# Kernel tuning notes

Hardware: AMD Instinct MI355X
Metric: run time of the kernel (lower is better)

## Reference

```python
import jax, jax.numpy as jnp
import numpy as np

GROUP = 64      # int4 quantization group size
QMAX = 7.0      # symmetric int4 grid [-8, 7], scales from max/7
EPS = 1e-6      # RMSNorm epsilon


def fake_quant_int4(t, group=GROUP):
    """Symmetric per-group int4 fake-quantization along the last dim (STE)."""
    shp = t.shape
    g = t.reshape(shp[:-1] + (shp[-1] // group, group))
    s = jnp.maximum(jnp.max(jnp.abs(g), axis=-1, keepdims=True) / QMAX, 1e-8)
    q = jnp.clip(jnp.round(g / s), -8.0, 7.0) * s
    out = g + jax.lax.stop_gradient(q - g)  # straight-through
    return out.reshape(shp)


def rms_norm(x, w):
    var = jnp.mean(jnp.square(x), axis=-1, keepdims=True)
    return x * jax.lax.rsqrt(var + EPS) * w


def apply_rope(x, cos, sin):
    # x: [B,S,H,D]; cos/sin: [S, D//2]; rotate consecutive pairs (complex mult)
    xr = x.reshape(x.shape[:-1] + (x.shape[-1] // 2, 2))
    a, b = xr[..., 0], xr[..., 1]
    c = cos[None, :, None, :]
    s = sin[None, :, None, :]
    out = jnp.stack([a * c - b * s, a * s + b * c], axis=-1)
    return out.reshape(x.shape)


def setup_inputs() -> dict:
    B, S, C, OUT, R, D = 2, 4096, 3072, 9216, 32, 128
    key = jax.random.key(0)
    ks = jax.random.split(key, 6)
    x = jax.random.normal(ks[0], (B, S, C), jnp.float32)
    smooth = jax.random.uniform(ks[1], (C,), jnp.float32, minval=0.5, maxval=1.5)
    weight = jax.random.normal(ks[2], (OUT, C), jnp.float32) * 0.02
    proj_down = jax.random.normal(ks[3], (C, R), jnp.float32) * 0.02
    proj_up = jax.random.normal(ks[4], (OUT, R), jnp.float32) * 0.02
    bias = jax.random.normal(ks[5], (OUT,), jnp.float32) * 0.01
    norm_q_weight = jnp.ones((D,), jnp.float32)
    norm_k_weight = jnp.ones((D,), jnp.float32)
    half = D // 2
    inv_freq = 1.0 / (10000.0 ** (jnp.arange(half, dtype=jnp.float32) / half))
    ang = jnp.arange(S, dtype=jnp.float32)[:, None] * inv_freq[None, :]
    return {
        "x": x, "smooth": smooth, "weight": weight,
        "proj_down": proj_down, "proj_up": proj_up, "bias": bias,
        "norm_q_weight": norm_q_weight, "norm_k_weight": norm_k_weight,
        "freqs_cos": jnp.cos(ang), "freqs_sin": jnp.sin(ang),
    }


def reference(x, smooth, weight, proj_down, proj_up, bias,
              norm_q_weight, norm_k_weight, freqs_cos, freqs_sin):
    B, S, C = x.shape
    OUT = weight.shape[0]
    D = norm_q_weight.shape[0]
    H = (OUT // 3) // D
    # --- svdq_quantize_w4a4_act_fuse_lora: smooth, lora-down, int4 quantize ---
    xs = x.reshape(B * S, C) / smooth                 # smoothed activations
    lora_act = xs @ proj_down                          # [BS, R]
    xq = fake_quant_int4(xs)                           # per-token group-64 int4
    # --- svdq_gemm_w4a4: int4 GEMM + LoRA-up + bias epilogue ---
    wq = fake_quant_int4(weight)                       # per-row group-64 int4
    out = xq @ wq.T + lora_act @ proj_up.T + bias      # [BS, OUT]
    out = out.reshape(B, S, 3, H, D)                   # q,k,v concat order
    q, k, v = out[:, :, 0], out[:, :, 1], out[:, :, 2]
    # --- fused RMSNorm + RoPE epilogue on q and k ---
    q = apply_rope(rms_norm(q, norm_q_weight), freqs_cos, freqs_sin)
    k = apply_rope(rms_norm(k, norm_k_weight), freqs_cos, freqs_sin)
    return jnp.concatenate(
        [q.reshape(B, S, -1), k.reshape(B, S, -1), v.reshape(B, S, -1)], axis=-1)
```

## Files before the change

kernel.cpp:

```cpp
#include <hip/hip_runtime.h>

#define CDIM  3072
#define MROWS 8192
#define NOUT  9216
#define NW    24

typedef __bf16 bf16x8 __attribute__((ext_vector_type(8)));
typedef float f32x4 __attribute__((ext_vector_type(4)));
typedef int i32x4 __attribute__((ext_vector_type(4)));

__device__ __forceinline__ unsigned short f2bf(float f) {
  union { float f; unsigned int u; } v; v.f = f;
  unsigned int u = v.u;
  return (unsigned short)((u + 0x7fffu + ((u >> 16) & 1u)) >> 16);
}
__device__ __forceinline__ float bfu_lo(unsigned int u) {
  union { unsigned int v; float f; } x; x.v = u << 16; return x.f;
}
__device__ __forceinline__ float bfu_hi(unsigned int u) {
  union { unsigned int v; float f; } x; x.v = u & 0xffff0000u; return x.f;
}
__device__ __forceinline__ void gld16(const void* g, void* l) {
  __builtin_amdgcn_global_load_lds(
      (const __attribute__((address_space(1))) void*)g,
      (__attribute__((address_space(3))) void*)l, 16, 0, 0);
}

#define BARRIER() asm volatile("s_barrier" ::: "memory")
#define LGKM0()   asm volatile("s_waitcnt lgkmcnt(0)" ::: "memory")

template<int N> __device__ __forceinline__ void vmw() {
  if constexpr (N == 8)      asm volatile("s_waitcnt vmcnt(8)" ::: "memory");
  else if constexpr (N == 4) asm volatile("s_waitcnt vmcnt(4)" ::: "memory");
  else if constexpr (N == 0) asm volatile("s_waitcnt vmcnt(0)" ::: "memory");
}

__device__ __forceinline__ unsigned int requant4(unsigned int u, float f) {
  const int q0 = (int)(signed char)(u & 0xff);
  const int q1 = (int)(signed char)((u >> 8) & 0xff);
  const int q2 = (int)(signed char)((u >> 16) & 0xff);
  const int q3 = (int)(signed char)(u >> 24);
  const int r0 = (int)rintf((float)q0 * f);
  const int r1 = (int)rintf((float)q1 * f);
  const int r2 = (int)rintf((float)q2 * f);
  const int r3 = (int)rintf((float)q3 * f);
  return (r0 & 0xff) | ((r1 & 0xff) << 8) | ((r2 & 0xff) << 16)
       | ((unsigned int)(r3 & 0xff) << 24);
}

__global__ __launch_bounds__(256) void k_prep(
    const float* __restrict__ wt, const float* __restrict__ pu,
    const float* __restrict__ x, const float* __restrict__ smooth,
    const float* __restrict__ pd,
    signed char* __restrict__ Bq, float* __restrict__ Sb_r,
    unsigned short* __restrict__ Blor,
    signed char* __restrict__ Aq, float* __restrict__ Sa_r,
    unsigned short* __restrict__ Alor) {
  __shared__ unsigned short xsb[4][3072];
  __shared__ float plds[4][32][33];
  __shared__ float sred[4];
  const int tid = threadIdx.x;

  if (blockIdx.x < NOUT) {
    const int row = blockIdx.x;
    unsigned int u[3]; float sl[3];
    #pragma unroll
    for (int it = 0; it < 3; ++it) {
      const int c = it * 1024 + tid * 4;
      const float4 v = *(const float4*)&wt[(size_t)row * CDIM + c];
      float am = fmaxf(fmaxf(fabsf(v.x), fabsf(v.y)), fmaxf(fabsf(v.z), fabsf(v.w)));
      #pragma unroll
      for (int off = 1; off < 16; off <<= 1) am = fmaxf(am, __shfl_xor(am, off));
      const float s = fmaxf(am / 7.0f, 1e-8f);
      union { signed char c[4]; unsigned int u; } pk;
      pk.c[0] = (signed char)(int)fminf(fmaxf(rintf(v.x / s), -8.f), 7.f);
      pk.c[1] = (signed char)(int)fminf(fmaxf(rintf(v.y / s), -8.f), 7.f);
      pk.c[2] = (signed char)(int)fminf(fmaxf(rintf(v.z / s), -8.f), 7.f);
      pk.c[3] = (signed char)(int)fminf(fmaxf(rintf(v.w / s), -8.f), 7.f);
      u[it] = pk.u; sl[it] = s;
    }
    float smax = fmaxf(fmaxf(sl[0], sl[1]), sl[2]);
    #pragma unroll
    for (int off = 16; off < 64; off <<= 1) smax = fmaxf(smax, __shfl_xor(smax, off));
    if ((tid & 63) == 0) sred[tid >> 6] = smax;
    __syncthreads();
    const float S = fmaxf(fmaxf(sred[0], sred[1]), fmaxf(sred[2], sred[3]));
    const float inv16 = 16.0f / S;
    #pragma unroll
    for (int it = 0; it < 3; ++it) {
      const int c = it * 1024 + tid * 4;
      *(unsigned int*)&Bq[(size_t)row * CDIM + c] = requant4(u[it], sl[it] * inv16);
    }
    if (tid == 0) Sb_r[row] = S * 0.0625f;
    if (tid < 32) Blor[row * 32 + tid] = f2bf(pu[row * 32 + tid]);
    return;
  }

  const int blk = blockIdx.x - NOUT;
  const int w = tid >> 6, l = tid & 63;
  const int row = blk * 4 + w;
  const float* xr = x + (size_t)row * CDIM;
  unsigned int u[12]; float sl[12];

  #pragma unroll
  for (int it = 0; it < 12; ++it) {
    const int c = it * 256 + l * 4;
    const float4 xv = *(const float4*)&xr[c];
    const float4 sm = *(const float4*)&smooth[c];
    float4 xs;
    xs.x = xv.x / sm.x; xs.y = xv.y / sm.y;
    xs.z = xv.z / sm.z; xs.w = xv.w / sm.w;
    ushort4 xb;
    xb.x = f2bf(xs.x); xb.y = f2bf(xs.y); xb.z = f2bf(xs.z); xb.w = f2bf(xs.w);
    *(ushort4*)&xsb[w][c] = xb;
    float am = fmaxf(fmaxf(fabsf(xs.x), fabsf(xs.y)), fmaxf(fabsf(xs.z), fabsf(xs.w)));
    #pragma unroll
    for (int off = 1; off < 16; off <<= 1) am = fmaxf(am, __shfl_xor(am, off));
    const float s = fmaxf(am / 7.0f, 1e-8f);
    union { signed char c[4]; unsigned int u; } pk;
    pk.c[0] = (signed char)(int)fminf(fmaxf(rintf(xs.x / s), -8.f), 7.f);
    pk.c[1] = (signed char)(int)fminf(fmaxf(rintf(xs.y / s), -8.f), 7.f);
    pk.c[2] = (signed char)(int)fminf(fmaxf(rintf(xs.z / s), -8.f), 7.f);
    pk.c[3] = (signed char)(int)fminf(fmaxf(rintf(xs.w / s), -8.f), 7.f);
    u[it] = pk.u; sl[it] = s;
  }
  float smax = sl[0];
  #pragma unroll
  for (int it = 1; it < 12; ++it) smax = fmaxf(smax, sl[it]);
  #pragma unroll
  for (int off = 16; off < 64; off <<= 1) smax = fmaxf(smax, __shfl_xor(smax, off));
  const float S = smax;
  const float inv16 = 16.0f / S;
  #pragma unroll
  for (int it = 0; it < 12; ++it) {
    const int c = it * 256 + l * 4;
    *(unsigned int*)&Aq[(size_t)row * CDIM + c] = requant4(u[it], sl[it] * inv16);
  }
  if (l == 0) Sa_r[row] = S * 0.0625f;
  __syncthreads();

  const int ch = tid >> 3, rg = tid & 7;
  float acc[4][4] = {};
  for (int i = 0; i < 48; ++i) {
    const int c = ch * 2 + i * 64;
    const float4 p0 = *(const float4*)&pd[(size_t)c * 32 + rg * 4];
    const float4 p1 = *(const float4*)&pd[(size_t)(c + 1) * 32 + rg * 4];
    #pragma unroll
    for (int r4 = 0; r4 < 4; ++r4) {
      const unsigned int uu = *(const unsigned int*)&xsb[r4][c];
      const float xa = bfu_lo(uu), xb = bfu_hi(uu);
      acc[r4][0] += xa * p0.x + xb * p1.x;
      acc[r4][1] += xa * p0.y + xb * p1.y;
      acc[r4][2] += xa * p0.z + xb * p1.z;
      acc[r4][3] += xa * p0.w + xb * p1.w;
    }
  }
  #pragma unroll
  for (int r4 = 0; r4 < 4; ++r4)
    #pragma unroll
    for (int jj = 0; jj < 4; ++jj)
      plds[r4][rg * 4 + jj][ch] = acc[r4][jj];
  __syncthreads();
  if (tid < 128) {
    const int rr = tid >> 5, r = tid & 31;
    float ssum = 0.f;
    #pragma unroll
    for (int cc = 0; cc < 32; ++cc) ssum += plds[rr][r][cc];
    Alor[(size_t)(blk * 4 + rr) * 32 + r] = f2bf(ssum);
  }
}

template<int VM1, int VM3, int DO01, int DO23>
__device__ __forceinline__ void gemm_window(
    char* lds, i32x4 (&acc)[8][4],
    const signed char* Asrc, const signed char* Bsrc,
    int tid, int arow, int brow, int fsb, int par, int t) {
  const int A0 = par * 16384;
  const int A1 = 32768 + par * 16384;
  const int B0 = 65536 + par * 16384;
  const int B1 = 98304 + par * 16384;
  const int A1n = 32768 + (par ^ 1) * 16384;
  const int B1n = 98304 + (par ^ 1) * 16384;
  i32x4 a[4], b[4];

  #pragma unroll
  for (int ni = 0; ni < 4; ++ni) b[ni] = *(const i32x4*)(lds + B0 + (brow + ni * 16) * 64 + fsb);
  #pragma unroll
  for (int mi = 0; mi < 4; ++mi) a[mi] = *(const i32x4*)(lds + A0 + (arow + mi * 16) * 64 + fsb);
  if (DO01) {
    const int kc = (t + 1) * 128 + 64;
    gld16(Asrc + kc, lds + A1n + tid * 16);
    gld16(Asrc + (size_t)128 * CDIM + kc, lds + A1n + 8192 + tid * 16);
  }
  BARRIER(); LGKM0();
  __builtin_amdgcn_s_setprio(1);
  #pragma unroll
  for (int mi = 0; mi < 4; ++mi)
    #pragma unroll
    for (int ni = 0; ni < 4; ++ni)
      acc[mi][ni] = __builtin_amdgcn_mfma_i32_16x16x64_i8(a[mi], b[ni], acc[mi][ni], 0, 0, 0);
  __builtin_amdgcn_s_setprio(0);
  BARRIER();

  #pragma unroll
  for (int mi = 0; mi < 4; ++mi) a[mi] = *(const i32x4*)(lds + A0 + (arow + 64 + mi * 16) * 64 + fsb);
  if (DO01) {
    const int kc = (t + 1) * 128 + 64;
    gld16(Bsrc + kc, lds + B1n + tid * 16);
    gld16(Bsrc + (size_t)128 * CDIM + kc, lds + B1n + 8192 + tid * 16);
  }
  BARRIER(); LGKM0();
  __builtin_amdgcn_s_setprio(1);
  #pragma unroll
  for (int mi = 0; mi < 4; ++mi)
    #pragma unroll
    for (int ni = 0; ni < 4; ++ni)
      acc[4 + mi][ni] = __builtin_amdgcn_mfma_i32_16x16x64_i8(a[mi], b[ni], acc[4 + mi][ni], 0, 0, 0);
  __builtin_amdgcn_s_setprio(0);
  vmw<VM1>();
  BARRIER();

  #pragma unroll
  for (int ni = 0; ni < 4; ++ni) b[ni] = *(const i32x4*)(lds + B1 + (brow + ni * 16) * 64 + fsb);
  #pragma unroll
  for (int mi = 0; mi < 4; ++mi) a[mi] = *(const i32x4*)(lds + A1 + (arow + mi * 16) * 64 + fsb);
  if (DO23) {
    const int kc = (t + 2) * 128;
    gld16(Asrc + kc, lds + A0 + tid * 16);
    gld16(Asrc + (size_t)128 * CDIM + kc, lds + A0 + 8192 + tid * 16);
  }
  BARRIER(); LGKM0();
  __builtin_amdgcn_s_setprio(1);
  #pragma unroll
  for (int mi = 0; mi < 4; ++mi)
    #pragma unroll
    for (int ni = 0; ni < 4; ++ni)
      acc[mi][ni] = __builtin_amdgcn_mfma_i32_16x16x64_i8(a[mi], b[ni], acc[mi][ni], 0, 0, 0);
  __builtin_amdgcn_s_setprio(0);
  BARRIER();

  #pragma unroll
  for (int mi = 0; mi < 4; ++mi) a[mi] = *(const i32x4*)(lds + A1 + (arow + 64 + mi * 16) * 64 + fsb);
  if (DO23) {
    const int kc = (t + 2) * 128;
    gld16(Bsrc + kc, lds + B0 + tid * 16);
    gld16(Bsrc + (size_t)128 * CDIM + kc, lds + B0 + 8192 + tid * 16);
  }
  BARRIER(); LGKM0();
  __builtin_amdgcn_s_setprio(1);
  #pragma unroll
  for (int mi = 0; mi < 4; ++mi)
    #pragma unroll
    for (int ni = 0; ni < 4; ++ni)
      acc[4 + mi][ni] = __builtin_amdgcn_mfma_i32_16x16x64_i8(a[mi], b[ni], acc[4 + mi][ni], 0, 0, 0);
  __builtin_amdgcn_s_setprio(0);
  vmw<VM3>();
  BARRIER();
}

__global__ __launch_bounds__(512, 2) void k_gemmi8(
    const signed char* __restrict__ Aq, const signed char* __restrict__ Bq,
    const float* __restrict__ Sa_r, const float* __restrict__ Sb_r,
    const unsigned short* __restrict__ Alor, const unsigned short* __restrict__ Blor,
    const float* __restrict__ bias,
    const float* __restrict__ nqw, const float* __restrict__ nkw,
    const float* __restrict__ fcos, const float* __restrict__ fsin,
    float* __restrict__ outp) {
  __shared__ char lds[131072];
  const int tid = threadIdx.x;
  const int w = tid >> 6, l = tid & 63;
  const int wr = w >> 2, wc = w & 3;
  const int l16 = l & 15, g16 = l >> 4;
  const int xcd = blockIdx.x & 7;
  const int jj = blockIdx.x >> 3;
  const int chunk = jj / 36;
  const int tt = jj - chunk * 36;
  const int by = xcd * 4 + tt / 9;
  const int bx = chunk * 9 + tt % 9;
  const int n0 = bx * 256, m0 = by * 256;
  const int arow = wr * 128 + l16;
  const int brow = wc * 64 + l16;
  const int fsb = (g16 ^ ((l16 >> 1) & 3)) << 4;
  const int sr = tid >> 2;
  const int ss = (((tid & 3) ^ ((sr >> 1) & 3)) << 4);
  const signed char* Asrc = Aq + (size_t)(m0 + sr) * CDIM + ss;
  const signed char* Bsrc = Bq + (size_t)(n0 + sr) * CDIM + ss;
  i32x4 acc[8][4] = {};

  gld16(Asrc, lds + tid * 16);                  gld16(Asrc + (size_t)128 * CDIM, lds + 8192 + tid * 16);
  gld16(Bsrc, lds + 65536 + tid * 16);          gld16(Bsrc + (size_t)128 * CDIM, lds + 73728 + tid * 16);
  gld16(Asrc + 64, lds + 32768 + tid * 16);     gld16(Asrc + (size_t)128 * CDIM + 64, lds + 40960 + tid * 16);
  gld16(Bsrc + 64, lds + 98304 + tid * 16);     gld16(Bsrc + (size_t)128 * CDIM + 64, lds + 106496 + tid * 16);
  gld16(Asrc + 128, lds + 16384 + tid * 16);    gld16(Asrc + (size_t)128 * CDIM + 128, lds + 24576 + tid * 16);
  gld16(Bsrc + 128, lds + 81920 + tid * 16);    gld16(Bsrc + (size_t)128 * CDIM + 128, lds + 90112 + tid * 16);
  vmw<8>(); BARRIER();

  #pragma unroll 1
  for (int t = 0; t <= NW - 3; ++t)
    gemm_window<8, 8, 1, 1>(lds, acc, Asrc, Bsrc, tid, arow, brow, fsb, t & 1, t);
  gemm_window<8, 4, 1, 0>(lds, acc, Asrc, Bsrc, tid, arow, brow, fsb, (NW - 2) & 1, NW - 2);
  gemm_window<0, 63, 0, 0>(lds, acc, Asrc, Bsrc, tid, arow, brow, fsb, (NW - 1) & 1, NW - 1);

  {
    const char* Al0 = (const char*)Alor + (size_t)(m0 + sr) * 64 + ss;
    const char* Bl0 = (const char*)Blor + (size_t)(n0 + sr) * 64 + ss;
    gld16(Al0, lds + tid * 16);            gld16(Al0 + 128 * 64, lds + 8192 + tid * 16);
    gld16(Bl0, lds + 65536 + tid * 16);    gld16(Bl0 + 128 * 64, lds + 73728 + tid * 16);
  }

  f32x4 facc[8][4];
  float sbv[4];
  #pragma unroll
  for (int ni = 0; ni < 4; ++ni) sbv[ni] = Sb_r[n0 + wc * 64 + ni * 16 + l16];
  #pragma unroll
  for (int q = 0; q < 8; ++q) {
    const f32x4 sa4 = *(const f32x4*)&Sa_r[m0 + wr * 128 + q * 16 + g16 * 4];
    #pragma unroll
    for (int ni = 0; ni < 4; ++ni)
      facc[q][ni] = __builtin_convertvector(acc[q][ni], f32x4) * (sa4 * sbv[ni]);
  }

  vmw<0>(); BARRIER();
  {
    bf16x8 bl[4];
    #pragma unroll
    for (int ni = 0; ni < 4; ++ni)
      bl[ni] = *(const bf16x8*)(lds + 65536 + (brow + ni * 16) * 64 + fsb);
    #pragma unroll
    for (int q = 0; q < 8; ++q) {
      const bf16x8 al = *(const bf16x8*)(lds + (arow + q * 16) * 64 + fsb);
      #pragma unroll
      for (int ni = 0; ni < 4; ++ni)
        facc[q][ni] = __builtin_amdgcn_mfma_f32_16x16x32_bf16(al, bl[ni], facc[q][ni], 0, 0, 0);
    }
  }

  float bvv[4];
  #pragma unroll
  for (int ni = 0; ni < 4; ++ni) bvv[ni] = bias[n0 + wc * 64 + ni * 16 + l16];
  #pragma unroll
  for (int q = 0; q < 8; ++q)
    #pragma unroll
    for (int ni = 0; ni < 4; ++ni)
      #pragma unroll
      for (int j = 0; j < 4; ++j) facc[q][ni][j] += bvv[ni];

  if (n0 < 6144) {
    const float* nwt = (n0 < 3072) ? nqw : nkw;
    float nw[4];
    #pragma unroll
    for (int ni = 0; ni < 4; ++ni) nw[ni] = nwt[(wc & 1) * 64 + ni * 16 + l16];

    float part[8][4];
    #pragma unroll
    for (int q = 0; q < 8; ++q)
      #pragma unroll
      for (int j = 0; j < 4; ++j) {
        float ssum = 0.f;
        #pragma unroll
        for (int ni = 0; ni < 4; ++ni) ssum += facc[q][ni][j] * facc[q][ni][j];
        #pragma unroll
        for (int off = 1; off < 16; off <<= 1) ssum += __shfl_xor(ssum, off);
        part[q][j] = ssum;
      }

    __syncthreads();
    float* sq = (float*)lds;
    if (l16 == 0) {
      #pragma unroll
      for (int q = 0; q < 8; ++q)
        #pragma unroll
        for (int j = 0; j < 4; ++j) {
          const int r128 = q * 16 + g16 * 4 + j;
          sq[(((wr * 128 + r128) * 2 + (wc >> 1)) * 2) + (wc & 1)] = part[q][j];
        }
    }
    __syncthreads();

    #pragma unroll
    for (int q = 0; q < 8; ++q) {
      #pragma unroll
      for (int j = 0; j < 4; ++j) {
        const int r128 = q * 16 + g16 * 4 + j;
        const float other = sq[(((wr * 128 + r128) * 2 + (wc >> 1)) * 2) + ((wc & 1) ^ 1)];
        const float rinv = 1.0f / sqrtf((part[q][j] + other) * (1.0f / 128.0f) + 1e-6f);
        const int row = m0 + wr * 128 + r128;
        const int sidx = row & 4095;
        #pragma unroll
        for (int ni = 0; ni < 4; ++ni) {
          const int p = (wc & 1) * 32 + ni * 8 + (l16 >> 1);
          const float cv = fcos[(size_t)sidx * 64 + p];
          const float sv = fsin[(size_t)sidx * 64 + p];
          const float v = facc[q][ni][j] * rinv * nw[ni];
          const float o = __shfl_xor(v, 1);
          const float res = ((l & 1) == 0) ? (v * cv - o * sv) : (o * sv + v * cv);
          __builtin_nontemporal_store(res, &outp[(size_t)row * NOUT + n0 + wc * 64 + ni * 16 + l16]);
        }
      }
    }
  } else {
    #pragma unroll
    for (int ni = 0; ni < 4; ++ni) {
      const int gn = n0 + wc * 64 + ni * 16 + l16;
      #pragma unroll
      for (int q = 0; q < 8; ++q) {
        const int gm = m0 + wr * 128 + q * 16 + g16 * 4;
        #pragma unroll
        for (int j = 0; j < 4; ++j)
          __builtin_nontemporal_store(facc[q][ni][j], &outp[(size_t)(gm + j) * NOUT + gn]);
      }
    }
  }
}

extern "C" void kernel_launch(void* const* d_in, const int* in_sizes, int n_in,
                              void* d_out, int out_size, void* d_ws, size_t ws_size,
                              hipStream_t stream) {
  const float* x      = (const float*)d_in[0];
  const float* smooth = (const float*)d_in[1];
  const float* weight = (const float*)d_in[2];
  const float* pd     = (const float*)d_in[3];
  const float* pu     = (const float*)d_in[4];
  const float* bias   = (const float*)d_in[5];
  const float* nqw    = (const float*)d_in[6];
  const float* nkw    = (const float*)d_in[7];
  const float* fcos   = (const float*)d_in[8];
  const float* fsin   = (const float*)d_in[9];
  float* out = (float*)d_out;

  char* ws = (char*)d_ws;
  signed char* Aq   = (signed char*)ws;
  signed char* Bq   = (signed char*)(ws + 25165824);
  float* Sa_r       = (float*)(ws + 53477376);
  float* Sb_r       = (float*)(ws + 53510144);
  unsigned short* Alor = (unsigned short*)(ws + 53547008);
  unsigned short* Blor = (unsigned short*)(ws + 54071296);

  k_prep<<<dim3(NOUT + MROWS / 4), dim3(256), 0, stream>>>(
      weight, pu, x, smooth, pd, Bq, Sb_r, Blor, Aq, Sa_r, Alor);
  k_gemmi8<<<dim3(1152), dim3(512), 0, stream>>>(Aq, Bq, Sa_r, Sb_r, Alor, Blor,
                                                 bias, nqw, nkw, fcos, fsin, out);
}
```

Measured before the change: 369.2 us.

## Restructure int8 GEMM main loop into two-phase double-buffered windows

The four-phase K window with staggered partial prefetches and `vmcnt(8)` waits is replaced by a two-phase window. Each phase reads both 64-wide K sub-tiles from LDS and issues two MFMAs per accumulator. All eight next-tile global loads are issued up front and drained with `vmcnt(0)` at the end of the window. The LoRA A/B tile loads are folded into the last window's prefetch slot. This halves the barriers per window and removes the separate epilogue wait, but the prefetch distance shrinks and the doubled a/b operand arrays raise register pressure.

Result: slower. 389.0 us (+5.4%).

```diff
diff --git a/kernel.cpp b/kernel.cpp
--- a/kernel.cpp
+++ b/kernel.cpp
@@ -30,9 +30,7 @@
 #define LGKM0()   asm volatile("s_waitcnt lgkmcnt(0)" ::: "memory")
 
 template<int N> __device__ __forceinline__ void vmw() {
-  if constexpr (N == 8)      asm volatile("s_waitcnt vmcnt(8)" ::: "memory");
-  else if constexpr (N == 4) asm volatile("s_waitcnt vmcnt(4)" ::: "memory");
-  else if constexpr (N == 0) asm volatile("s_waitcnt vmcnt(0)" ::: "memory");
+  if constexpr (N == 0) asm volatile("s_waitcnt vmcnt(0)" ::: "memory");
 }
 
 __device__ __forceinline__ unsigned int requant4(unsigned int u, float f) {
@@ -170,91 +168,75 @@
   }
 }
 
-template<int VM1, int VM3, int DO01, int DO23>
-__device__ __forceinline__ void gemm_window(
+__device__ __forceinline__ void gemm_window2(
     char* lds, i32x4 (&acc)[8][4],
     const signed char* Asrc, const signed char* Bsrc,
-    int tid, int arow, int brow, int fsb, int par, int t) {
+    const char* AlorP, const char* BlorP,
+    int tid, int arow, int brow, int fsb, int par, int t, int mode) {
   const int A0 = par * 16384;
   const int A1 = 32768 + par * 16384;
   const int B0 = 65536 + par * 16384;
   const int B1 = 98304 + par * 16384;
+  const int A0n = (par ^ 1) * 16384;
   const int A1n = 32768 + (par ^ 1) * 16384;
+  const int B0n = 65536 + (par ^ 1) * 16384;
   const int B1n = 98304 + (par ^ 1) * 16384;
-  i32x4 a[4], b[4];
-
-  #pragma unroll
-  for (int ni = 0; ni < 4; ++ni) b[ni] = *(const i32x4*)(lds + B0 + (brow + ni * 16) * 64 + fsb);
-  #pragma unroll
-  for (int mi = 0; mi < 4; ++mi) a[mi] = *(const i32x4*)(lds + A0 + (arow + mi * 16) * 64 + fsb);
-  if (DO01) {
-    const int kc = (t + 1) * 128 + 64;
-    gld16(Asrc + kc, lds + A1n + tid * 16);
-    gld16(Asrc + (size_t)128 * CDIM + kc, lds + A1n + 8192 + tid * 16);
+  i32x4 a[8], b[8];
+
+  #pragma unroll
+  for (int ni = 0; ni < 4; ++ni) {
+    b[ni]     = *(const i32x4*)(lds + B0 + (brow + ni * 16) * 64 + fsb);
+    b[4 + ni] = *(const i32x4*)(lds + B1 + (brow + ni * 16) * 64 + fsb);
+  }
+  #pragma unroll
+  for (int mi = 0; mi < 4; ++mi) {
+    a[mi]     = *(const i32x4*)(lds + A0 + (arow + mi * 16) * 64 + fsb);
+    a[4 + mi] = *(const i32x4*)(lds + A1 + (arow + mi * 16) * 64 + fsb);
+  }
+  if (mode == 0) {
+    const int kc = (t + 1) * 128;
+    gld16(Asrc + kc,                            lds + A0n + tid * 16);
+    gld16(Asrc + (size_t)128 * CDIM + kc,       lds + A0n + 8192 + tid * 16);
+    gld16(Asrc + kc + 64,                       lds + A1n + tid * 16);
+    gld16(Asrc + (size_t)128 * CDIM + kc + 64,  lds + A1n + 8192 + tid * 16);
+    gld16(Bsrc + kc,                            lds + B0n + tid * 16);
+    gld16(Bsrc + (size_t)128 * CDIM + kc,       lds + B0n + 8192 + tid * 16);
+    gld16(Bsrc + kc + 64,                       lds + B1n + tid * 16);
+    gld16(Bsrc + (size_t)128 * CDIM + kc + 64,  lds + B1n + 8192 + tid * 16);
+  } else if (mode == 1) {
+    gld16(AlorP,            lds + A0n + tid * 16);
+    gld16(AlorP + 128 * 64, lds + A0n + 8192 + tid * 16);
+    gld16(BlorP,            lds + B0n + tid * 16);
+    gld16(BlorP + 128 * 64, lds + B0n + 8192 + tid * 16);
   }
   BARRIER(); LGKM0();
   __builtin_amdgcn_s_setprio(1);
   #pragma unroll
   for (int mi = 0; mi < 4; ++mi)
     #pragma unroll
-    for (int ni = 0; ni < 4; ++ni)
+    for (int ni = 0; ni < 4; ++ni) {
       acc[mi][ni] = __builtin_amdgcn_mfma_i32_16x16x64_i8(a[mi], b[ni], acc[mi][ni], 0, 0, 0);
+      acc[mi][ni] = __builtin_amdgcn_mfma_i32_16x16x64_i8(a[4 + mi], b[4 + ni], acc[mi][ni], 0, 0, 0);
+    }
   __builtin_amdgcn_s_setprio(0);
   BARRIER();
 
   #pragma unroll
-  for (int mi = 0; mi < 4; ++mi) a[mi] = *(const i32x4*)(lds + A0 + (arow + 64 + mi * 16) * 64 + fsb);
-  if (DO01) {
-    const int kc = (t + 1) * 128 + 64;
-    gld16(Bsrc + kc, lds + B1n + tid * 16);
-    gld16(Bsrc + (size_t)128 * CDIM + kc, lds + B1n + 8192 + tid * 16);
+  for (int mi = 0; mi < 4; ++mi) {
+    a[mi]     = *(const i32x4*)(lds + A0 + (arow + 64 + mi * 16) * 64 + fsb);
+    a[4 + mi] = *(const i32x4*)(lds + A1 + (arow + 64 + mi * 16) * 64 + fsb);
   }
   BARRIER(); LGKM0();
   __builtin_amdgcn_s_setprio(1);
   #pragma unroll
   for (int mi = 0; mi < 4; ++mi)
     #pragma unroll
-    for (int ni = 0; ni < 4; ++ni)
+    for (int ni = 0; ni < 4; ++ni) {
       acc[4 + mi][ni] = __builtin_amdgcn_mfma_i32_16x16x64_i8(a[mi], b[ni], acc[4 + mi][ni], 0, 0, 0);
+      acc[4 + mi][ni] = __builtin_amdgcn_mfma_i32_16x16x64_i8(a[4 + mi], b[4 + ni], acc[4 + mi][ni], 0, 0, 0);
+    }
   __builtin_amdgcn_s_setprio(0);
-  vmw<VM1>();
-  BARRIER();
-
-  #pragma unroll
-  for (int ni = 0; ni < 4; ++ni) b[ni] = *(const i32x4*)(lds + B1 + (brow + ni * 16) * 64 + fsb);
-  #pragma unroll
-  for (int mi = 0; mi < 4; ++mi) a[mi] = *(const i32x4*)(lds + A1 + (arow + mi * 16) * 64 + fsb);
-  if (DO23) {
-    const int kc = (t + 2) * 128;
-    gld16(Asrc + kc, lds + A0 + tid * 16);
-    gld16(Asrc + (size_t)128 * CDIM + kc, lds + A0 + 8192 + tid * 16);
-  }
-  BARRIER(); LGKM0();
-  __builtin_amdgcn_s_setprio(1);
-  #pragma unroll
-  for (int mi = 0; mi < 4; ++mi)
-    #pragma unroll
-    for (int ni = 0; ni < 4; ++ni)
-      acc[mi][ni] = __builtin_amdgcn_mfma_i32_16x16x64_i8(a[mi], b[ni], acc[mi][ni], 0, 0, 0);
-  __builtin_amdgcn_s_setprio(0);
-  BARRIER();
-
-  #pragma unroll
-  for (int mi = 0; mi < 4; ++mi) a[mi] = *(const i32x4*)(lds + A1 + (arow + 64 + mi * 16) * 64 + fsb);
-  if (DO23) {
-    const int kc = (t + 2) * 128;
-    gld16(Bsrc + kc, lds + B0 + tid * 16);
-    gld16(Bsrc + (size_t)128 * CDIM + kc, lds + B0 + 8192 + tid * 16);
-  }
-  BARRIER(); LGKM0();
-  __builtin_amdgcn_s_setprio(1);
-  #pragma unroll
-  for (int mi = 0; mi < 4; ++mi)
-    #pragma unroll
-    for (int ni = 0; ni < 4; ++ni)
-      acc[4 + mi][ni] = __builtin_amdgcn_mfma_i32_16x16x64_i8(a[mi], b[ni], acc[4 + mi][ni], 0, 0, 0);
-  __builtin_amdgcn_s_setprio(0);
-  vmw<VM3>();
+  vmw<0>();
   BARRIER();
 }
 
@@ -285,28 +267,24 @@
   const int ss = (((tid & 3) ^ ((sr >> 1) & 3)) << 4);
   const signed char* Asrc = Aq + (size_t)(m0 + sr) * CDIM + ss;
   const signed char* Bsrc = Bq + (size_t)(n0 + sr) * CDIM + ss;
+  const char* AlorP = (const char*)Alor + (size_t)(m0 + sr) * 64 + ss;
+  const char* BlorP = (const char*)Blor + (size_t)(n0 + sr) * 64 + ss;
   i32x4 acc[8][4] = {};
 
-  gld16(Asrc, lds + tid * 16);                  gld16(Asrc + (size_t)128 * CDIM, lds + 8192 + tid * 16);
-  gld16(Bsrc, lds + 65536 + tid * 16);          gld16(Bsrc + (size_t)128 * CDIM, lds + 73728 + tid * 16);
-  gld16(Asrc + 64, lds + 32768 + tid * 16);     gld16(Asrc + (size_t)128 * CDIM + 64, lds + 40960 + tid * 16);
-  gld16(Bsrc + 64, lds + 98304 + tid * 16);     gld16(Bsrc + (size_t)128 * CDIM + 64, lds + 106496 + tid * 16);
-  gld16(Asrc + 128, lds + 16384 + tid * 16);    gld16(Asrc + (size_t)128 * CDIM + 128, lds + 24576 + tid * 16);
-  gld16(Bsrc + 128, lds + 81920 + tid * 16);    gld16(Bsrc + (size_t)128 * CDIM + 128, lds + 90112 + tid * 16);
-  vmw<8>(); BARRIER();
+  gld16(Asrc,                           lds + tid * 16);
+  gld16(Asrc + (size_t)128 * CDIM,      lds + 8192 + tid * 16);
+  gld16(Asrc + 64,                      lds + 32768 + tid * 16);
+  gld16(Asrc + (size_t)128 * CDIM + 64, lds + 40960 + tid * 16);
+  gld16(Bsrc,                           lds + 65536 + tid * 16);
+  gld16(Bsrc + (size_t)128 * CDIM,      lds + 73728 + tid * 16);
+  gld16(Bsrc + 64,                      lds + 98304 + tid * 16);
+  gld16(Bsrc + (size_t)128 * CDIM + 64, lds + 106496 + tid * 16);
+  vmw<0>(); BARRIER();
 
   #pragma unroll 1
-  for (int t = 0; t <= NW - 3; ++t)
-    gemm_window<8, 8, 1, 1>(lds, acc, Asrc, Bsrc, tid, arow, brow, fsb, t & 1, t);
-  gemm_window<8, 4, 1, 0>(lds, acc, Asrc, Bsrc, tid, arow, brow, fsb, (NW - 2) & 1, NW - 2);
-  gemm_window<0, 63, 0, 0>(lds, acc, Asrc, Bsrc, tid, arow, brow, fsb, (NW - 1) & 1, NW - 1);
-
-  {
-    const char* Al0 = (const char*)Alor + (size_t)(m0 + sr) * 64 + ss;
-    const char* Bl0 = (const char*)Blor + (size_t)(n0 + sr) * 64 + ss;
-    gld16(Al0, lds + tid * 16);            gld16(Al0 + 128 * 64, lds + 8192 + tid * 16);
-    gld16(Bl0, lds + 65536 + tid * 16);    gld16(Bl0 + 128 * 64, lds + 73728 + tid * 16);
-  }
+  for (int t = 0; t < NW - 1; ++t)
+    gemm_window2(lds, acc, Asrc, Bsrc, AlorP, BlorP, tid, arow, brow, fsb, t & 1, t, 0);
+  gemm_window2(lds, acc, Asrc, Bsrc, AlorP, BlorP, tid, arow, brow, fsb, (NW - 1) & 1, NW - 1, 1);
 
   f32x4 facc[8][4];
   float sbv[4];
@@ -320,7 +298,6 @@
       facc[q][ni] = __builtin_convertvector(acc[q][ni], f32x4) * (sa4 * sbv[ni]);
   }
 
-  vmw<0>(); BARRIER();
   {
     bf16x8 bl[4];
     #pragma unroll
```
